# Optimization experiments

Hardware: AMD Instinct MI355X
Metric: run time of the kernel (lower is better)

## Reference

```python
import jax, jax.numpy as jnp
import numpy as np

B, MAX_N, MAX_E, MAX_BETA = 16, 512, 1024, 64
NODE_F, HID = 2, 128

def setup_inputs() -> dict:
    key = jax.random.key(0)
    ks = jax.random.split(key, 20)
    inp = {}
    inp["x"] = jax.random.normal(ks[0], (B, MAX_N, NODE_F), dtype=jnp.float32)
    inp["SCB"] = jax.random.normal(ks[1], (B, MAX_BETA, MAX_E), dtype=jnp.float32)
    inp["edge_index"] = jax.random.randint(ks[2], (B, 2, MAX_E), 0, MAX_N, dtype=jnp.int32)
    inp["edge_len"] = jax.random.randint(ks[3], (B,), 1, MAX_E + 1, dtype=jnp.int32)
    inp["beta_len"] = jax.random.randint(ks[4], (B,), 1, MAX_BETA + 1, dtype=jnp.int32)
    def lin(k, fi, fo):
        s = 1.0 / np.sqrt(fi)
        kw, kb = jax.random.split(k)
        return (jax.random.uniform(kw, (fi, fo), jnp.float32, -s, s),
                jax.random.uniform(kb, (fo,), jnp.float32, -s, s))
    inp["W1"], inp["b1"] = lin(ks[5], 4, 64)
    inp["W2"], inp["b2"] = lin(ks[6], 64, 64)
    inp["W3"], inp["b3"] = lin(ks[7], 64 + 4, 128)
    inp["W4"], inp["b4"] = lin(ks[8], 128, 128)
    inp["W5"], inp["b5"] = lin(ks[9], 128, HID)
    inp["W6"], inp["b6"] = lin(ks[10], HID, HID)
    return inp

def reference(x, SCB, edge_index, edge_len, beta_len,
              W1, b1, W2, b2, W3, b3, W4, b4, W5, b5, W6, b6):
    Bb, beta, E = SCB.shape
    SCBa = jnp.abs(SCB)  # torch.abs(he[2].to_dense())
    edge_mask = jnp.arange(E)[None, :] < edge_len[:, None]      # [B,E]
    beta_mask = jnp.arange(beta)[None, :] < beta_len[:, None]   # [B,beta]
    # e_feat = x[edge_index].transpose(0,1).reshape(E, 2*node_feat)
    ef = jax.vmap(lambda xi, ei: xi[ei])(x, edge_index)          # [B,2,E,F]
    ef = jnp.transpose(ef, (0, 2, 1, 3)).reshape(Bb, E, -1)      # [B,E,4]
    # SCB_feat[b,beta,e,i] = e_feat[b,e,i] * SCB[b,beta,e]; zero in padded region
    valid = (beta_mask[:, :, None] & edge_mask[:, None, :])[..., None]
    SCB_feat = jnp.where(valid, SCBa[:, :, :, None] * ef[:, None, :, :], 0.0)  # [B,beta,E,4]
    L1 = jnp.transpose(SCB_feat, (0, 2, 1, 3))                   # [B,E,beta,4]
    # SCB_encoder on sum over edges
    s = L1.sum(axis=1)                                            # [B,beta,4]
    emb = jax.nn.relu(s @ W1 + b1) @ W2 + b2                      # [B,beta,64]
    cat = jnp.concatenate([jnp.broadcast_to(emb[:, None], (Bb, E, beta, 64)), L1], axis=-1)
    h = (jax.nn.relu(cat @ W3 + b3) @ W4 + b4).sum(axis=2)        # [B,E,128]
    out = jax.nn.relu(h @ W5 + b5) @ W6 + b6                      # [B,E,HID]
    out = out.reshape(Bb * E, -1)
    # original selects out[Pad_Masks]; zero padded rows instead (jit-static shape)
    return out * edge_mask.reshape(-1, 1).astype(out.dtype)
```

## Files before the change

kernel.cpp:

```cpp
#include <hip/hip_runtime.h>
#include <hip/hip_bf16.h>

#define NB   16
#define NN   512
#define NE   1024
#define NBETA 64
#define NHID 128

typedef __attribute__((ext_vector_type(8))) short short8;
typedef __attribute__((ext_vector_type(4))) float f32x4;

static __device__ __forceinline__ unsigned short f2bf(float f) {
    unsigned u = __float_as_uint(f);
    return (unsigned short)((u + 0x7fffu + ((u >> 16) & 1u)) >> 16);
}

static __device__ __forceinline__ f32x4 splat4(float v) {
    f32x4 r; r.x = v; r.y = v; r.z = v; r.w = v; return r;
}


__global__ __launch_bounds__(128) void k_base_wt(
        const float* __restrict__ x, const int* __restrict__ ei,
        const float* __restrict__ SCB,
        const int* __restrict__ elen, const int* __restrict__ blen,
        const float* __restrict__ W1, const float* __restrict__ b1,
        const float* __restrict__ W2, const float* __restrict__ b2,
        const float* __restrict__ W3, const float* __restrict__ b3,
        const float* __restrict__ W4, const float* __restrict__ W5,
        const float* __restrict__ W6,
        float* __restrict__ base, unsigned short* __restrict__ wsT) {
    int bid = blockIdx.x, tid = threadIdx.x;
    if (bid >= NB * NBETA) {
        int j = (bid - NB * NBETA) * 128 + tid;
        int w = j >> 14, rem = j & 16383;
        int k = rem & 127, n = rem >> 7;
        const float* W = (w == 0) ? W4 : ((w == 1) ? W5 : W6);
        float v = W[k * NHID + n];
        int byte = n * 256 + ((2 * k) ^ ((n & 7) << 4));
        *reinterpret_cast<unsigned short*>(
            reinterpret_cast<char*>(wsT) + (size_t)w * 32768 + byte) = f2bf(v);
        return;
    }
    int bb = bid;
    int b = bb >> 6, beta = bb & 63;
    int el = elen[b], bl = blen[b];
    float a0 = 0, a1 = 0, a2 = 0, a3 = 0;
    if (beta < bl) {
        const float* row = SCB + (size_t)bb * NE;
        const int* eis = ei + b * 2 * NE;
        const float* xb = x + b * NN * 2;
        for (int e = tid; e < el; e += 128) {
            float t = fabsf(row[e]);
            int s0 = eis[e], s1 = eis[NE + e];
            float2 v0 = *reinterpret_cast<const float2*>(xb + 2 * s0);
            float2 v1 = *reinterpret_cast<const float2*>(xb + 2 * s1);
            a0 = fmaf(t, v0.x, a0);
            a1 = fmaf(t, v0.y, a1);
            a2 = fmaf(t, v1.x, a2);
            a3 = fmaf(t, v1.y, a3);
        }
    }
    __shared__ float red[4][128];
    red[0][tid] = a0; red[1][tid] = a1; red[2][tid] = a2; red[3][tid] = a3;
    __syncthreads();
    for (int st = 64; st > 0; st >>= 1) {
        if (tid < st) {
            red[0][tid] += red[0][tid + st];
            red[1][tid] += red[1][tid + st];
            red[2][tid] += red[2][tid + st];
            red[3][tid] += red[3][tid + st];
        }
        __syncthreads();
    }
    __shared__ float h1[64], embv[64];
    if (tid < 64) {
        float v = b1[tid];
        #pragma unroll
        for (int i = 0; i < 4; ++i) v = fmaf(red[i][0], W1[i * 64 + tid], v);
        h1[tid] = fmaxf(v, 0.f);
    }
    __syncthreads();
    if (tid < 64) {
        float v = b2[tid];
        #pragma unroll 8
        for (int k = 0; k < 64; ++k) v = fmaf(h1[k], W2[k * 64 + tid], v);
        embv[tid] = v;
    }
    __syncthreads();
    float v = b3[tid];
    #pragma unroll 8
    for (int k = 0; k < 64; ++k) v = fmaf(embv[k], W3[k * NHID + tid], v);
    base[(size_t)bb * NHID + tid] = v;
}

__global__ __launch_bounds__(512) void k_fused(
        const float* __restrict__ x, const int* __restrict__ ei,
        const float* __restrict__ SCB,
        const int* __restrict__ elen, const int* __restrict__ blen,
        const float* __restrict__ W3,
        const float* __restrict__ base, const unsigned short* __restrict__ wsT,
        const float* __restrict__ b4, const float* __restrict__ b5,
        const float* __restrict__ b6,
        float* __restrict__ out) {
    __shared__ __align__(16) char regionA[49152];
    __shared__ __align__(16) char ioA[16384];
    int bid = blockIdx.x, tid = threadIdx.x;
    int b = bid >> 4;
    int e0 = (bid & 15) * 64;
    int el = elen[b], bl = blen[b];

    float* baseS = reinterpret_cast<float*>(regionA);
    float* tS    = reinterpret_cast<float*>(regionA + 32768);
    float4* efS  = reinterpret_cast<float4*>(ioA);
    float* w3r   = reinterpret_cast<float*>(ioA + 1024);

    {
        const float4* bsrc = reinterpret_cast<const float4*>(base + (size_t)b * NBETA * NHID);
        float4* bd = reinterpret_cast<float4*>(baseS);
        for (int i = tid; i < NBETA * NHID / 4; i += 512) bd[i] = bsrc[i];
        for (int i = tid; i < NBETA * 16; i += 512) {
            int row = i >> 4, c4 = i & 15;
            float4 v = *reinterpret_cast<const float4*>(
                SCB + ((size_t)(b * NBETA + row)) * NE + e0 + c4 * 4);
            v.x = fabsf(v.x); v.y = fabsf(v.y); v.z = fabsf(v.z); v.w = fabsf(v.w);
            reinterpret_cast<float4*>(tS)[i] = v;
        }
        if (tid < 128) {
            int e = tid >> 1, hf = tid & 1;
            int idx = ei[b * 2 * NE + hf * NE + e0 + e];
            float2 v = *reinterpret_cast<const float2*>(x + b * NN * 2 + idx * 2);
            reinterpret_cast<float2*>(&efS[e])[hf] = v;
        }
        w3r[tid] = W3[64 * NHID + tid];
    }
    __syncthreads();

    int cg = tid & 31, slot = tid >> 5;
    f32x4 w0  = reinterpret_cast<const f32x4*>(w3r)[0 * 32 + cg];
    f32x4 w1  = reinterpret_cast<const f32x4*>(w3r)[1 * 32 + cg];
    f32x4 w2  = reinterpret_cast<const f32x4*>(w3r)[2 * 32 + cg];
    f32x4 w3v = reinterpret_cast<const f32x4*>(w3r)[3 * 32 + cg];
    f32x4 gv[4], acc[4];
    #pragma unroll
    for (int j = 0; j < 4; ++j) {
        float4 e4 = efS[slot * 4 + j];
        f32x4 g = w3v * splat4(e4.w);
        g = __builtin_elementwise_fma(splat4(e4.z), w2, g);
        g = __builtin_elementwise_fma(splat4(e4.y), w1, g);
        g = __builtin_elementwise_fma(splat4(e4.x), w0, g);
        gv[j] = g;
        acc[j] = splat4(0.f);
    }
    __syncthreads();

    const f32x4* base4 = reinterpret_cast<const f32x4*>(baseS);
    const float4* t4 = reinterpret_cast<const float4*>(tS);
    const f32x4 zero = splat4(0.f);
    for (int beta = 0; beta < bl; ++beta) {
        f32x4 bs = base4[beta * 32 + cg];
        float4 tv = t4[beta * 16 + slot];
        acc[0] += __builtin_elementwise_max(__builtin_elementwise_fma(splat4(tv.x), gv[0], bs), zero);
        acc[1] += __builtin_elementwise_max(__builtin_elementwise_fma(splat4(tv.y), gv[1], bs), zero);
        acc[2] += __builtin_elementwise_max(__builtin_elementwise_fma(splat4(tv.z), gv[2], bs), zero);
        acc[3] += __builtin_elementwise_max(__builtin_elementwise_fma(splat4(tv.w), gv[3], bs), zero);
    }
    if (bl < NBETA) {
        f32x4 bp = base4[bl * 32 + cg];
        f32x4 r = __builtin_elementwise_max(bp, zero);
        f32x4 fcv = splat4((float)(NBETA - bl));
        #pragma unroll
        for (int j = 0; j < 4; ++j) acc[j] = __builtin_elementwise_fma(fcv, r, acc[j]);
    }
    #pragma unroll
    for (int j = 0; j < 4; ++j) {
        int rl = slot * 4 + j;
        int byte = rl * 256 + ((cg * 8) ^ ((rl & 7) << 4));
        ushort4 u;
        u.x = f2bf(acc[j].x); u.y = f2bf(acc[j].y);
        u.z = f2bf(acc[j].z); u.w = f2bf(acc[j].w);
        *reinterpret_cast<ushort4*>(ioA + byte) = u;
    }

    int l = tid & 63, wid = tid >> 6;
    int wm = wid & 3, wn = wid >> 2;
    const int lrow = l & 15;
    const int kbl = (l >> 4) * 16;
    char* wS = regionA;
    char* ioB = regionA + 32768;

    auto layer = [&](const char* ioIn, char* ioOut, int widx, const float* bias,
                     float bscale, bool doRelu, bool final_) {
        __syncthreads();
        {
            const float4* wsrc = reinterpret_cast<const float4*>(
                reinterpret_cast<const char*>(wsT) + (size_t)widx * 32768);
            float4* wd = reinterpret_cast<float4*>(wS);
            for (int i = tid; i < 2048; i += 512) wd[i] = wsrc[i];
        }
        __syncthreads();

        f32x4 facc[4];
        #pragma unroll
        for (int nf = 0; nf < 4; ++nf) facc[nf] = splat4(0.f);
        int rowA = wm * 16 + lrow;
        #pragma unroll
        for (int ks = 0; ks < 4; ++ks) {
            int kbyte = ks * 64 + kbl;
            short8 a = *reinterpret_cast<const short8*>(
                ioIn + rowA * 256 + (kbyte ^ ((rowA & 7) << 4)));
            #pragma unroll
            for (int nf = 0; nf < 4; ++nf) {
                int col = wn * 64 + nf * 16 + lrow;
                short8 bf = *reinterpret_cast<const short8*>(
                    wS + col * 256 + (kbyte ^ ((col & 7) << 4)));
                facc[nf] = __builtin_amdgcn_mfma_f32_16x16x32_bf16(a, bf, facc[nf], 0, 0, 0);
            }
        }
        #pragma unroll
        for (int nf = 0; nf < 4; ++nf) {
            int colg = wn * 64 + nf * 16 + lrow;
            float bv = bias[colg];
            #pragma unroll
            for (int r = 0; r < 4; ++r) {
                int row = wm * 16 + (l >> 4) * 4 + r;
                float v = fmaf(bscale, bv, facc[nf][r]);
                if (doRelu) v = fmaxf(v, 0.f);
                if (!final_) {
                    *reinterpret_cast<unsigned short*>(
                        ioOut + row * 256 + ((colg * 2) ^ ((row & 7) << 4))) = f2bf(v);
                } else {
                    int rg = bid * 64 + row;
                    if ((rg & (NE - 1)) >= el) v = 0.f;
                    out[(size_t)rg * NHID + colg] = v;
                }
            }
        }
    };

    layer(ioA, ioB, 0, b4, 64.f, false, false);
    layer(ioB, ioA, 1, b5, 1.f, true, false);
    layer(ioA, nullptr, 2, b6, 1.f, false, true);
}

extern "C" void kernel_launch(void* const* d_in, const int* in_sizes, int n_in,
                              void* d_out, int out_size, void* d_ws, size_t ws_size,
                              hipStream_t stream) {
    const float* x    = (const float*)d_in[0];
    const float* SCB  = (const float*)d_in[1];
    const int*   ei   = (const int*)d_in[2];
    const int*   elen = (const int*)d_in[3];
    const int*   blen = (const int*)d_in[4];
    const float* W1 = (const float*)d_in[5];  const float* b1 = (const float*)d_in[6];
    const float* W2 = (const float*)d_in[7];  const float* b2 = (const float*)d_in[8];
    const float* W3 = (const float*)d_in[9];  const float* b3 = (const float*)d_in[10];
    const float* W4 = (const float*)d_in[11]; const float* b4 = (const float*)d_in[12];
    const float* W5 = (const float*)d_in[13]; const float* b5 = (const float*)d_in[14];
    const float* W6 = (const float*)d_in[15]; const float* b6 = (const float*)d_in[16];
    float* out = (float*)d_out;

    float* ws = (float*)d_ws;
    float* base = ws;
    unsigned short* wsT = (unsigned short*)(base + NB * NBETA * NHID);

    hipLaunchKernelGGL(k_base_wt, dim3(NB * NBETA + 384), dim3(128), 0, stream,
                       x, ei, SCB, elen, blen, W1, b1, W2, b2, W3, b3, W4, W5, W6, base, wsT);
    hipLaunchKernelGGL(k_fused, dim3(256), dim3(512), 0, stream,
                       x, ei, SCB, elen, blen, W3, base, wsT, b4, b5, b6, out);
}
```

Baseline: 29.38 us.

## Halve edge tile, skip padded tiles, prefetch next layer weights into registers

```diff
diff --git a/kernel.cpp b/kernel.cpp
--- a/kernel.cpp
+++ b/kernel.cpp
@@ -103,48 +103,68 @@
         const float* __restrict__ b4, const float* __restrict__ b5,
         const float* __restrict__ b6,
         float* __restrict__ out) {
-    __shared__ __align__(16) char regionA[49152];
-    __shared__ __align__(16) char ioA[16384];
     int bid = blockIdx.x, tid = threadIdx.x;
-    int b = bid >> 4;
-    int e0 = (bid & 15) * 64;
-    int el = elen[b], bl = blen[b];
-
-    float* baseS = reinterpret_cast<float*>(regionA);
-    float* tS    = reinterpret_cast<float*>(regionA + 32768);
-    float4* efS  = reinterpret_cast<float4*>(ioA);
-    float* w3r   = reinterpret_cast<float*>(ioA + 1024);
+    int b = bid >> 5;
+    int e0 = (bid & 31) * 32;
+    int el = elen[b];
+    if (e0 >= el) {
+        float4 z; z.x = 0.f; z.y = 0.f; z.z = 0.f; z.w = 0.f;
+        float4* o4 = reinterpret_cast<float4*>(out) + (size_t)(b * NE + e0) * (NHID / 4);
+        o4[tid] = z;
+        o4[tid + 512] = z;
+        return;
+    }
+    int bl = blen[b];
+
+    __shared__ __align__(16) char lds[65536];
+    float* baseS = reinterpret_cast<float*>(lds);
+    char*  wS    = lds + 32768;
+    float4* efS  = reinterpret_cast<float4*>(wS);
+    float* w3r   = reinterpret_cast<float*>(wS + 512);
+    float* tS    = reinterpret_cast<float*>(wS + 8192);
+    char* io0 = lds;
+    char* io1 = lds + 8192;
+
+    const float4* w4src = reinterpret_cast<const float4*>(wsT);
+    const float4* w5src = reinterpret_cast<const float4*>(
+        reinterpret_cast<const char*>(wsT) + 32768);
+    const float4* w6src = reinterpret_cast<const float4*>(
+        reinterpret_cast<const char*>(wsT) + 65536);
+    float4 pw0, pw1, pw2, pw3;
 
     {
         const float4* bsrc = reinterpret_cast<const float4*>(base + (size_t)b * NBETA * NHID);
         float4* bd = reinterpret_cast<float4*>(baseS);
-        for (int i = tid; i < NBETA * NHID / 4; i += 512) bd[i] = bsrc[i];
-        for (int i = tid; i < NBETA * 16; i += 512) {
-            int row = i >> 4, c4 = i & 15;
+        #pragma unroll
+        for (int i = 0; i < 4; ++i) bd[tid + 512 * i] = bsrc[tid + 512 * i];
+        {
+            int row = tid >> 3, c4 = tid & 7;
             float4 v = *reinterpret_cast<const float4*>(
-                SCB + ((size_t)(b * NBETA + row)) * NE + e0 + c4 * 4);
+                SCB + (size_t)(b * NBETA + row) * NE + e0 + c4 * 4);
             v.x = fabsf(v.x); v.y = fabsf(v.y); v.z = fabsf(v.z); v.w = fabsf(v.w);
-            reinterpret_cast<float4*>(tS)[i] = v;
-        }
-        if (tid < 128) {
+            reinterpret_cast<float4*>(tS)[tid] = v;
+        }
+        if (tid < 64) {
             int e = tid >> 1, hf = tid & 1;
             int idx = ei[b * 2 * NE + hf * NE + e0 + e];
-            float2 v = *reinterpret_cast<const float2*>(x + b * NN * 2 + idx * 2);
-            reinterpret_cast<float2*>(&efS[e])[hf] = v;
+            float2 v2 = *reinterpret_cast<const float2*>(x + b * NN * 2 + idx * 2);
+            reinterpret_cast<float2*>(&efS[e])[hf] = v2;
         }
         w3r[tid] = W3[64 * NHID + tid];
-    }
-    __syncthreads();
-
-    int cg = tid & 31, slot = tid >> 5;
-    f32x4 w0  = reinterpret_cast<const f32x4*>(w3r)[0 * 32 + cg];
-    f32x4 w1  = reinterpret_cast<const f32x4*>(w3r)[1 * 32 + cg];
-    f32x4 w2  = reinterpret_cast<const f32x4*>(w3r)[2 * 32 + cg];
-    f32x4 w3v = reinterpret_cast<const f32x4*>(w3r)[3 * 32 + cg];
-    f32x4 gv[4], acc[4];
+        pw0 = w4src[tid];        pw1 = w4src[tid + 512];
+        pw2 = w4src[tid + 1024]; pw3 = w4src[tid + 1536];
+    }
+    __syncthreads();
+
+    int cg = tid & 31, es = tid >> 5;
+    f32x4 w0  = reinterpret_cast<const f32x4*>(w3r)[cg];
+    f32x4 w1  = reinterpret_cast<const f32x4*>(w3r)[32 + cg];
+    f32x4 w2  = reinterpret_cast<const f32x4*>(w3r)[64 + cg];
+    f32x4 w3v = reinterpret_cast<const f32x4*>(w3r)[96 + cg];
+    f32x4 gv[2], acc[2];
     #pragma unroll
-    for (int j = 0; j < 4; ++j) {
-        float4 e4 = efS[slot * 4 + j];
+    for (int j = 0; j < 2; ++j) {
+        float4 e4 = efS[es * 2 + j];
         f32x4 g = w3v * splat4(e4.w);
         g = __builtin_elementwise_fma(splat4(e4.z), w2, g);
         g = __builtin_elementwise_fma(splat4(e4.y), w1, g);
@@ -152,57 +172,50 @@
         gv[j] = g;
         acc[j] = splat4(0.f);
     }
-    __syncthreads();
-
     const f32x4* base4 = reinterpret_cast<const f32x4*>(baseS);
-    const float4* t4 = reinterpret_cast<const float4*>(tS);
     const f32x4 zero = splat4(0.f);
     for (int beta = 0; beta < bl; ++beta) {
         f32x4 bs = base4[beta * 32 + cg];
-        float4 tv = t4[beta * 16 + slot];
-        acc[0] += __builtin_elementwise_max(__builtin_elementwise_fma(splat4(tv.x), gv[0], bs), zero);
-        acc[1] += __builtin_elementwise_max(__builtin_elementwise_fma(splat4(tv.y), gv[1], bs), zero);
-        acc[2] += __builtin_elementwise_max(__builtin_elementwise_fma(splat4(tv.z), gv[2], bs), zero);
-        acc[3] += __builtin_elementwise_max(__builtin_elementwise_fma(splat4(tv.w), gv[3], bs), zero);
+        float2 tv = *reinterpret_cast<const float2*>(tS + beta * 32 + es * 2);
+        acc[0] += __builtin_elementwise_max(
+            __builtin_elementwise_fma(splat4(tv.x), gv[0], bs), zero);
+        acc[1] += __builtin_elementwise_max(
+            __builtin_elementwise_fma(splat4(tv.y), gv[1], bs), zero);
     }
     if (bl < NBETA) {
         f32x4 bp = base4[bl * 32 + cg];
         f32x4 r = __builtin_elementwise_max(bp, zero);
         f32x4 fcv = splat4((float)(NBETA - bl));
-        #pragma unroll
-        for (int j = 0; j < 4; ++j) acc[j] = __builtin_elementwise_fma(fcv, r, acc[j]);
-    }
+        acc[0] = __builtin_elementwise_fma(fcv, r, acc[0]);
+        acc[1] = __builtin_elementwise_fma(fcv, r, acc[1]);
+    }
+    __syncthreads();
+
     #pragma unroll
-    for (int j = 0; j < 4; ++j) {
-        int rl = slot * 4 + j;
+    for (int j = 0; j < 2; ++j) {
+        int rl = es * 2 + j;
         int byte = rl * 256 + ((cg * 8) ^ ((rl & 7) << 4));
         ushort4 u;
+        u.x = f2bf(acc[0][0]);
         u.x = f2bf(acc[j].x); u.y = f2bf(acc[j].y);
         u.z = f2bf(acc[j].z); u.w = f2bf(acc[j].w);
-        *reinterpret_cast<ushort4*>(ioA + byte) = u;
-    }
+        *reinterpret_cast<ushort4*>(io0 + byte) = u;
+    }
+    float4* wd = reinterpret_cast<float4*>(wS);
+    wd[tid] = pw0; wd[tid + 512] = pw1; wd[tid + 1024] = pw2; wd[tid + 1536] = pw3;
+    pw0 = w5src[tid];        pw1 = w5src[tid + 512];
+    pw2 = w5src[tid + 1024]; pw3 = w5src[tid + 1536];
+    __syncthreads();
 
     int l = tid & 63, wid = tid >> 6;
-    int wm = wid & 3, wn = wid >> 2;
+    int wm = wid & 1, wn = wid >> 1;
     const int lrow = l & 15;
     const int kbl = (l >> 4) * 16;
-    char* wS = regionA;
-    char* ioB = regionA + 32768;
-
-    auto layer = [&](const char* ioIn, char* ioOut, int widx, const float* bias,
-                     float bscale, bool doRelu, bool final_) {
-        __syncthreads();
-        {
-            const float4* wsrc = reinterpret_cast<const float4*>(
-                reinterpret_cast<const char*>(wsT) + (size_t)widx * 32768);
-            float4* wd = reinterpret_cast<float4*>(wS);
-            for (int i = tid; i < 2048; i += 512) wd[i] = wsrc[i];
-        }
-        __syncthreads();
-
-        f32x4 facc[4];
-        #pragma unroll
-        for (int nf = 0; nf < 4; ++nf) facc[nf] = splat4(0.f);
+
+    auto layerc = [&](const char* ioIn, char* ioOut, const float* bias,
+                      float bscale, bool doRelu, bool final_) {
+        f32x4 facc[2];
+        facc[0] = splat4(0.f); facc[1] = splat4(0.f);
         int rowA = wm * 16 + lrow;
         #pragma unroll
         for (int ks = 0; ks < 4; ++ks) {
@@ -210,37 +223,45 @@
             short8 a = *reinterpret_cast<const short8*>(
                 ioIn + rowA * 256 + (kbyte ^ ((rowA & 7) << 4)));
             #pragma unroll
-            for (int nf = 0; nf < 4; ++nf) {
-                int col = wn * 64 + nf * 16 + lrow;
+            for (int nf = 0; nf < 2; ++nf) {
+                int col = wn * 32 + nf * 16 + lrow;
                 short8 bf = *reinterpret_cast<const short8*>(
                     wS + col * 256 + (kbyte ^ ((col & 7) << 4)));
                 facc[nf] = __builtin_amdgcn_mfma_f32_16x16x32_bf16(a, bf, facc[nf], 0, 0, 0);
             }
         }
         #pragma unroll
-        for (int nf = 0; nf < 4; ++nf) {
-            int colg = wn * 64 + nf * 16 + lrow;
-            float bv = bias[colg];
+        for (int nf = 0; nf < 2; ++nf) {
+            int colg = wn * 32 + nf * 16 + lrow;
+            float bvv = bias[colg];
             #pragma unroll
             for (int r = 0; r < 4; ++r) {
                 int row = wm * 16 + (l >> 4) * 4 + r;
-                float v = fmaf(bscale, bv, facc[nf][r]);
+                float v = fmaf(bscale, bvv, facc[nf][r]);
                 if (doRelu) v = fmaxf(v, 0.f);
                 if (!final_) {
                     *reinterpret_cast<unsigned short*>(
                         ioOut + row * 256 + ((colg * 2) ^ ((row & 7) << 4))) = f2bf(v);
                 } else {
-                    int rg = bid * 64 + row;
-                    if ((rg & (NE - 1)) >= el) v = 0.f;
-                    out[(size_t)rg * NHID + colg] = v;
+                    int eg = e0 + row;
+                    if (eg >= el) v = 0.f;
+                    out[(size_t)(b * NE + eg) * NHID + colg] = v;
                 }
             }
         }
     };
 
-    layer(ioA, ioB, 0, b4, 64.f, false, false);
-    layer(ioB, ioA, 1, b5, 1.f, true, false);
-    layer(ioA, nullptr, 2, b6, 1.f, false, true);
+    layerc(io0, io1, b4, 64.f, false, false);
+    __syncthreads();
+    wd[tid] = pw0; wd[tid + 512] = pw1; wd[tid + 1024] = pw2; wd[tid + 1536] = pw3;
+    pw0 = w6src[tid];        pw1 = w6src[tid + 512];
+    pw2 = w6src[tid + 1024]; pw3 = w6src[tid + 1536];
+    __syncthreads();
+    layerc(io1, io0, b5, 1.f, true, false);
+    __syncthreads();
+    wd[tid] = pw0; wd[tid + 512] = pw1; wd[tid + 1024] = pw2; wd[tid + 1536] = pw3;
+    __syncthreads();
+    layerc(io0, nullptr, b6, 1.f, false, true);
 }
 
 extern "C" void kernel_launch(void* const* d_in, const int* in_sizes, int n_in,
@@ -265,6 +286,6 @@
 
     hipLaunchKernelGGL(k_base_wt, dim3(NB * NBETA + 384), dim3(128), 0, stream,
                        x, ei, SCB, elen, blen, W1, b1, W2, b2, W3, b3, W4, W5, W6, base, wsT);
-    hipLaunchKernelGGL(k_fused, dim3(256), dim3(512), 0, stream,
+    hipLaunchKernelGGL(k_fused, dim3(512), dim3(512), 0, stream,
                        x, ei, SCB, elen, blen, W3, base, wsT, b4, b5, b6, out);
 }
```

Result: faster. 26.96 us (-8.2%).
